# Optimization experiments

Measured on AMD Instinct MI355X. Metric: run time of the kernel, lower is better.

## Reference

```python
import jax, jax.numpy as jnp
import numpy as np

N = 100000   # nodes
E = 3200000  # edges
G = 256      # graphs in batch
C_IN, H, OUT = 5, 64, 2
EPS = 1e-5


def setup_inputs() -> dict:
    key = jax.random.key(0)
    ks = jax.random.split(key, 16)
    d = {
        "x": jax.random.normal(ks[0], (N, C_IN), jnp.float32),
        "edge_index": jax.random.randint(ks[1], (2, E), 0, N, jnp.int64),
        "batch": jnp.sort(jax.random.randint(ks[2], (N,), 0, G, jnp.int64)),
        "W1": jax.random.normal(ks[3], (C_IN, H), jnp.float32),
        "b1": jax.random.normal(ks[4], (H,), jnp.float32),
        "g1": jax.random.uniform(ks[5], (H,), jnp.float32),
        "be1": jax.random.normal(ks[6], (H,), jnp.float32),
        "rm1": jnp.zeros((H,), jnp.float32),
        "rv1": jnp.ones((H,), jnp.float32),
        "W2": jax.random.normal(ks[7], (H, H), jnp.float32),
        "b2": jax.random.normal(ks[8], (H,), jnp.float32),
        "g2": jax.random.uniform(ks[9], (H,), jnp.float32),
        "be2": jax.random.normal(ks[10], (H,), jnp.float32),
        "rm2": jnp.zeros((H,), jnp.float32),
        "rv2": jnp.ones((H,), jnp.float32),
        "W3": jax.random.normal(ks[11], (H, H), jnp.float32),
        "b3": jax.random.normal(ks[12], (H,), jnp.float32),
        "g3": jax.random.uniform(ks[13], (H,), jnp.float32),
        "be3": jax.random.normal(ks[14], (H,), jnp.float32),
        "rm3": jnp.zeros((H,), jnp.float32),
        "rv3": jnp.ones((H,), jnp.float32),
        "Wf1": jax.random.normal(ks[15], (H, 32), jnp.float32),
        "bf1": jax.random.normal(jax.random.fold_in(key, 1), (32,), jnp.float32),
        "Wf2": jax.random.normal(jax.random.fold_in(key, 2), (32, OUT), jnp.float32),
        "bf2": jax.random.normal(jax.random.fold_in(key, 3), (OUT,), jnp.float32),
    }
    return d


def reference(x, edge_index, batch, W1, b1, g1, be1, rm1, rv1,
              W2, b2, g2, be2, rm2, rv2, W3, b3, g3, be3, rm3, rv3,
              Wf1, bf1, Wf2, bf2):
    src, dst = edge_index[0], edge_index[1]
    # GCN symmetric normalization with self-loops: deg includes the self edge
    deg = jax.ops.segment_sum(jnp.ones((E,), x.dtype), dst, num_segments=N) + 1.0
    dinv = jax.lax.rsqrt(deg)            # [N]
    enorm = dinv[src] * dinv[dst]        # per-edge norm  [E]
    snorm = dinv * dinv                  # self-loop norm [N]

    def gcn(h, W, b):
        h = h @ W                                                  # [N,H]
        agg = jax.ops.segment_sum(h[src] * enorm[:, None], dst, num_segments=N)
        return agg + h * snorm[:, None] + b

    def bn(h, g, be, rm, rv):  # eval-mode BatchNorm1d
        return (h - rm) * jax.lax.rsqrt(rv + EPS) * g + be

    h = jax.nn.relu(bn(gcn(x, W1, b1), g1, be1, rm1, rv1))
    h = jax.nn.relu(bn(gcn(h, W2, b2), g2, be2, rm2, rv2))
    h = jax.nn.relu(bn(gcn(h, W3, b3), g3, be3, rm3, rv3))

    counts = jax.ops.segment_sum(jnp.ones((N,), h.dtype), batch, num_segments=G)
    pooled = jax.ops.segment_sum(h, batch, num_segments=G) / jnp.maximum(counts, 1.0)[:, None]

    h = jax.nn.relu(pooled @ Wf1 + bf1)  # dropout is identity in eval
    return jax.nn.sigmoid(h @ Wf2 + bf2)
```

## Files before the change

### kernel.cpp

```cpp
#include <hip/hip_runtime.h>
#include <hip/hip_bf16.h>

#define HF 64
#define EPS 1e-5f

#define BSH 9
#define BKN (1 << BSH)
#define NBUCK_MAX 256
#define PB_T 256
#define PB_EPT 32
#define PB_TILE (PB_T * PB_EPT)

#define LGRID 2048

typedef __hip_bfloat16 bf16;

__device__ __forceinline__ unsigned char f32_to_fp8(float v) {
    int p = __builtin_amdgcn_cvt_pk_fp8_f32(v, v, 0, false);
    return (unsigned char)(p & 0xff);
}

__device__ __forceinline__ float rdlane(float v, int k) {
    return __int_as_float(__builtin_amdgcn_readlane(__float_as_int(v), k));
}

__device__ __forceinline__ unsigned bf16_rne_hi(float x) {
    unsigned u = __float_as_uint(x);
    return (u + 0x7fffu + ((u >> 16) & 1u)) & 0xffff0000u;
}

__global__ __launch_bounds__(PB_T) void k_passB2(
    const int* __restrict__ src, const int* __restrict__ dst,
    int* __restrict__ stage, unsigned* __restrict__ rtab,
    int* __restrict__ bcnt, int E, int B) {
    __shared__ int scnt[NBUCK_MAX];
    __shared__ int sscan[PB_T];
    int t = threadIdx.x;
    int blk = blockIdx.x;
    int tile0 = blk * PB_TILE;

    for (int b = t; b < NBUCK_MAX; b += PB_T) scnt[b] = 0;
    __syncthreads();

    int rec[PB_EPT];
    int bkt[PB_EPT];
#pragma unroll
    for (int k = 0; k < PB_EPT; ++k) {
        int e = tile0 + k * PB_T + t;
        bkt[k] = -1;
        if (e < E) {
            int d = dst[e];
            int s = src[e];
            int b = d >> BSH;
            bkt[k] = b;
            rec[k] = s | ((d & (BKN - 1)) << 17);
            atomicAdd(&scnt[b], 1);
        }
    }
    __syncthreads();

    int v = (t < B) ? scnt[t] : 0;
    sscan[t] = v;
    __syncthreads();
    for (int off = 1; off < PB_T; off <<= 1) {
        int val = sscan[t];
        int add = (t >= off) ? sscan[t - off] : 0;
        __syncthreads();
        sscan[t] = val + add;
        __syncthreads();
    }
    int excl = sscan[t] - v;
    if (t < B) {
        rtab[(size_t)blk * B + t] = ((unsigned)excl << 14) | (unsigned)v;
        scnt[t] = excl;
        if (v) atomicAdd(&bcnt[t], v);
    }
    __syncthreads();

#pragma unroll
    for (int k = 0; k < PB_EPT; ++k) {
        if (bkt[k] >= 0) {
            int loc = atomicAdd(&scnt[bkt[k]], 1);
            stage[tile0 + loc] = rec[k];
        }
    }
}

__global__ void k_bscan3(const int* __restrict__ bcnt, int* __restrict__ bbase2,
                         int* __restrict__ base, int B, int N, int E) {
    __shared__ int tot[NBUCK_MAX];
    int t = threadIdx.x;
    int v = (t < B) ? bcnt[t] : 0;
    tot[t] = v;
    __syncthreads();
    for (int off = 1; off < 256; off <<= 1) {
        int val = tot[t];
        int add = (t >= off) ? tot[t - off] : 0;
        __syncthreads();
        tot[t] = val + add;
        __syncthreads();
    }
    if (t < B) bbase2[t] = tot[t] - v;
    if (t == 0) { bbase2[B] = E; base[N] = E; }
}

__global__ __launch_bounds__(512) void k_passC2(const int* __restrict__ stage,
                                                const unsigned* __restrict__ rtab,
                                                const int* __restrict__ bb2,
                                                const float* __restrict__ x,
                                                int* __restrict__ base,
                                                float* __restrict__ dinv,
                                                float* __restrict__ xs,
                                                int* __restrict__ csr,
                                                int N, int B, int nblk) {
    __shared__ int lcnt[BKN];
    __shared__ int lscan[BKN];
    __shared__ int lcur[BKN];
    int beta = blockIdx.x;
    int n0 = beta * BKN;
    int n1 = n0 + BKN; if (n1 > N) n1 = N;
    int nn = n1 - n0;
    int t = threadIdx.x;
    int rg = t >> 4;
    int le = t & 15;
    lcnt[t] = 0;
    __syncthreads();

    for (int blk0 = 0; blk0 < nblk; blk0 += 32) {
        int blk = blk0 + rg;
        if (blk < nblk) {
            unsigned rt = rtab[(size_t)blk * B + beta];
            int cnt = (int)(rt & 0x3FFFu);
            int off = blk * PB_TILE + (int)(rt >> 14);
            for (int i = le; i < cnt; i += 16)
                atomicAdd(&lcnt[stage[off + i] >> 17], 1);
        }
    }
    __syncthreads();
    int v = lcnt[t];
    lscan[t] = v;
    __syncthreads();
    for (int off = 1; off < 512; off <<= 1) {
        int val = lscan[t];
        int add = (t >= off) ? lscan[t - off] : 0;
        __syncthreads();
        lscan[t] = val + add;
        __syncthreads();
    }
    int b = bb2[beta] + lscan[t] - v;
    if (t < nn) {
        int n = n0 + t;
        float di = rsqrtf((float)v + 1.0f);
        base[n] = b;
        dinv[n] = di;
#pragma unroll
        for (int c2 = 0; c2 < 5; ++c2)
            xs[n * 5 + c2] = x[n * 5 + c2] * di;
    }
    lcur[t] = b;
    __syncthreads();

    for (int blk0 = 0; blk0 < nblk; blk0 += 32) {
        int blk = blk0 + rg;
        if (blk < nblk) {
            unsigned rt = rtab[(size_t)blk * B + beta];
            int cnt = (int)(rt & 0x3FFFu);
            int off = blk * PB_TILE + (int)(rt >> 14);
            for (int i = le; i < cnt; i += 16) {
                int r = stage[off + i];
                int pos = atomicAdd(&lcur[r >> 17], 1);
                csr[pos] = r & 0x1ffff;
            }
        }
    }
}

__global__ __launch_bounds__(256) void k_layer1(
    const float* __restrict__ xs, unsigned char* __restrict__ hout,
    const int* __restrict__ csr, const int* __restrict__ basep,
    const float* __restrict__ dinv,
    const float* __restrict__ W1, const float* __restrict__ b,
    const float* __restrict__ g, const float* __restrict__ be,
    const float* __restrict__ rm, const float* __restrict__ rv, int N) {
    __shared__ float sW[5 * HF];
    __shared__ float sB[HF];
    __shared__ float sScale[HF];
    if (threadIdx.x < HF) {
        int f = threadIdx.x;
        float scale = g[f] * rsqrtf(rv[f] + EPS);
        sScale[f] = scale;
        sB[f] = (b[f] - rm[f]) * scale + be[f];
    }
    __syncthreads();
    for (int i = threadIdx.x; i < 5 * HF; i += blockDim.x)
        sW[i] = W1[i] * sScale[i & (HF - 1)];
    __syncthreads();

    int lane = threadIdx.x & 63;
    int wave = threadIdx.x >> 6;
    int c  = lane & 7;
    int g8 = lane >> 3;
    int stride = gridDim.x * 4;

    auto mlp_store = [&](float accS, int nodeS, float diS) {
        float out = sB[lane];
#pragma unroll
        for (int k = 0; k < 5; ++k) out += __shfl(accS, k, 64) * sW[k * HF + lane];
        out = fmaxf(out, 0.f);
        hout[(size_t)nodeS * HF + lane] = f32_to_fp8(out * diS);
    };

    float accP = 0.f, diP = 0.f;
    int nodeP = -1;

    for (int node = blockIdx.x * 4 + wave; node < N; node += stride) {
        int j   = __builtin_amdgcn_readfirstlane(basep[node]);
        int end = __builtin_amdgcn_readfirstlane(basep[node + 1]);

        float a0 = 0.f, a1 = 0.f, a2 = 0.f, a3 = 0.f;
        if (g8 == 0 && c < 5) a0 = xs[node * 5 + c];

        float u0 = 0.f, u1 = 0.f, u2 = 0.f, u3 = 0.f;
        bool w0 = (j + 32 <= end);
        if (w0) {
            int s0 = csr[j + g8];
            int s1 = csr[j + 8 + g8];
            int s2 = csr[j + 16 + g8];
            int s3 = csr[j + 24 + g8];
            u0 = xs[s0 * 5 + c]; u1 = xs[s1 * 5 + c];
            u2 = xs[s2 * 5 + c]; u3 = xs[s3 * 5 + c];
        }

        if (nodeP >= 0) mlp_store(accP, nodeP, diP);

        if (w0) {
            j += 32;
            while (j + 32 <= end) {
                int s0 = csr[j + g8];
                int s1 = csr[j + 8 + g8];
                int s2 = csr[j + 16 + g8];
                int s3 = csr[j + 24 + g8];
                float v0 = xs[s0 * 5 + c];
                float v1 = xs[s1 * 5 + c];
                float v2 = xs[s2 * 5 + c];
                float v3 = xs[s3 * 5 + c];
                a0 += u0; a1 += u1; a2 += u2; a3 += u3;
                u0 = v0; u1 = v1; u2 = v2; u3 = v3;
                j += 32;
            }
            a0 += u0; a1 += u1; a2 += u2; a3 += u3;
        }
        for (; j + 8 <= end; j += 8) {
            int s = csr[j + g8];
            a0 += xs[s * 5 + c];
        }
        if (j < end && j + g8 < end) {
            int s = csr[j + g8];
            a0 += xs[s * 5 + c];
        }

        float acc = (a0 + a1) + (a2 + a3);
        acc += __shfl_xor(acc, 8, 64);
        acc += __shfl_xor(acc, 16, 64);
        acc += __shfl_xor(acc, 32, 64);

        float di = dinv[node];
        accP = acc * di;
        diP = di;
        nodeP = node;
    }
    if (nodeP >= 0) mlp_store(accP, nodeP, diP);
}

template <int SCALE_OUT>
__global__ __launch_bounds__(256, 4) void k_layer(
    const unsigned char* __restrict__ hs8, void* __restrict__ hout_v,
    const int* __restrict__ csr, const int* __restrict__ basep,
    const float* __restrict__ dinv,
    const float* __restrict__ W, const float* __restrict__ b,
    const float* __restrict__ g, const float* __restrict__ be,
    const float* __restrict__ rm, const float* __restrict__ rv, int N) {
    __shared__ uint4 swp4[64][9];

    int lane = threadIdx.x & 63;
    int wave = threadIdx.x >> 6;
    int stride = gridDim.x * 4;
    const unsigned char* col = hs8 + lane;

    if (threadIdx.x < 64) {
        int l = threadIdx.x;
        float sc = g[l] * rsqrtf(rv[l] + EPS);
#pragma unroll
        for (int c = 0; c < 8; ++c) {
            unsigned p[4];
#pragma unroll
            for (int q = 0; q < 4; ++q) {
                int k2 = c * 4 + q;
                unsigned lo = bf16_rne_hi(W[(2 * k2 + 0) * HF + l] * sc);
                unsigned hi = bf16_rne_hi(W[(2 * k2 + 1) * HF + l] * sc);
                p[q] = (lo >> 16) | hi;
            }
            swp4[l][c] = make_uint4(p[0], p[1], p[2], p[3]);
        }
    }
    __syncthreads();

    float scale = g[lane] * rsqrtf(rv[lane] + EPS);
    float bias  = (b[lane] - rm[lane]) * scale + be[lane];

    auto mlp_store = [&](float acc, int nodeS, float diS) {
        float o0 = bias, o1 = 0.f, o2 = 0.f, o3 = 0.f;
#pragma unroll
        for (int c = 0; c < 8; ++c) {
            uint4 pv = swp4[lane][c];
            int k0 = c * 8;
            o0 += rdlane(acc, k0 + 0) * __uint_as_float(pv.x << 16);
            o1 += rdlane(acc, k0 + 1) * __uint_as_float(pv.x & 0xffff0000u);
            o2 += rdlane(acc, k0 + 2) * __uint_as_float(pv.y << 16);
            o3 += rdlane(acc, k0 + 3) * __uint_as_float(pv.y & 0xffff0000u);
            o0 += rdlane(acc, k0 + 4) * __uint_as_float(pv.z << 16);
            o1 += rdlane(acc, k0 + 5) * __uint_as_float(pv.z & 0xffff0000u);
            o2 += rdlane(acc, k0 + 6) * __uint_as_float(pv.w << 16);
            o3 += rdlane(acc, k0 + 7) * __uint_as_float(pv.w & 0xffff0000u);
        }
        float out = fmaxf((o0 + o1) + (o2 + o3), 0.f);
        if (SCALE_OUT) {
            ((unsigned char*)hout_v)[(size_t)nodeS * HF + lane] = f32_to_fp8(out * diS);
        } else {
            ((unsigned short*)hout_v)[(size_t)nodeS * HF + lane] =
                (unsigned short)(bf16_rne_hi(out) >> 16);
        }
    };

    float accP = 0.f, diP = 0.f;
    int nodeP = -1;

    for (int node = blockIdx.x * 4 + wave; node < N; node += stride) {
        int j   = __builtin_amdgcn_readfirstlane(basep[node]);
        int end = __builtin_amdgcn_readfirstlane(basep[node + 1]);

        float a0 = __builtin_amdgcn_cvt_f32_fp8((unsigned)col[(size_t)node * HF], 0);
        float a1 = 0.f, a2 = 0.f, a3 = 0.f;

        unsigned u0 = 0, u1 = 0, u2 = 0, u3 = 0, u4 = 0, u5 = 0, u6 = 0, u7 = 0;
        bool w0 = (j + 8 <= end);
        if (w0) {
            int s0 = csr[j+0], s1 = csr[j+1], s2 = csr[j+2], s3 = csr[j+3];
            int s4 = csr[j+4], s5 = csr[j+5], s6 = csr[j+6], s7 = csr[j+7];
            u0 = col[(size_t)s0 * HF]; u1 = col[(size_t)s1 * HF];
            u2 = col[(size_t)s2 * HF]; u3 = col[(size_t)s3 * HF];
            u4 = col[(size_t)s4 * HF]; u5 = col[(size_t)s5 * HF];
            u6 = col[(size_t)s6 * HF]; u7 = col[(size_t)s7 * HF];
        }

        if (nodeP >= 0) mlp_store(accP, nodeP, diP);

        if (w0) {
            j += 8;
            while (j + 8 <= end) {
                int t0 = csr[j+0], t1 = csr[j+1], t2 = csr[j+2], t3 = csr[j+3];
                int t4 = csr[j+4], t5 = csr[j+5], t6 = csr[j+6], t7 = csr[j+7];
                unsigned v0 = col[(size_t)t0 * HF];
                unsigned v1 = col[(size_t)t1 * HF];
                unsigned v2 = col[(size_t)t2 * HF];
                unsigned v3 = col[(size_t)t3 * HF];
                unsigned v4 = col[(size_t)t4 * HF];
                unsigned v5 = col[(size_t)t5 * HF];
                unsigned v6 = col[(size_t)t6 * HF];
                unsigned v7 = col[(size_t)t7 * HF];
                a0 += __builtin_amdgcn_cvt_f32_fp8(u0, 0);
                a1 += __builtin_amdgcn_cvt_f32_fp8(u1, 0);
                a2 += __builtin_amdgcn_cvt_f32_fp8(u2, 0);
                a3 += __builtin_amdgcn_cvt_f32_fp8(u3, 0);
                a0 += __builtin_amdgcn_cvt_f32_fp8(u4, 0);
                a1 += __builtin_amdgcn_cvt_f32_fp8(u5, 0);
                a2 += __builtin_amdgcn_cvt_f32_fp8(u6, 0);
                a3 += __builtin_amdgcn_cvt_f32_fp8(u7, 0);
                u0 = v0; u1 = v1; u2 = v2; u3 = v3;
                u4 = v4; u5 = v5; u6 = v6; u7 = v7;
                j += 8;
            }
            a0 += __builtin_amdgcn_cvt_f32_fp8(u0, 0);
            a1 += __builtin_amdgcn_cvt_f32_fp8(u1, 0);
            a2 += __builtin_amdgcn_cvt_f32_fp8(u2, 0);
            a3 += __builtin_amdgcn_cvt_f32_fp8(u3, 0);
            a0 += __builtin_amdgcn_cvt_f32_fp8(u4, 0);
            a1 += __builtin_amdgcn_cvt_f32_fp8(u5, 0);
            a2 += __builtin_amdgcn_cvt_f32_fp8(u6, 0);
            a3 += __builtin_amdgcn_cvt_f32_fp8(u7, 0);
        }
        for (; j < end; ++j) {
            int s = csr[j];
            a0 += __builtin_amdgcn_cvt_f32_fp8((unsigned)col[(size_t)s * HF], 0);
        }

        float di = dinv[node];
        accP = ((a0 + a1) + (a2 + a3)) * di;
        diP = di;
        nodeP = node;
    }
    if (nodeP >= 0) mlp_store(accP, nodeP, diP);
}

__global__ void k_pool_fc(const unsigned short* __restrict__ h, const int* __restrict__ batch,
                          const float* __restrict__ Wf1, const float* __restrict__ bf1,
                          const float* __restrict__ Wf2, const float* __restrict__ bf2,
                          float* __restrict__ out, int N) {
    int g = blockIdx.x;
    int t = threadIdx.x;
    int f = t & 63, q = t >> 6;

    int lo = 0, hi = N;
    while (lo < hi) { int mid = (lo + hi) >> 1; if (batch[mid] < g) lo = mid + 1; else hi = mid; }
    int start = lo;
    hi = N;
    while (lo < hi) { int mid = (lo + hi) >> 1; if (batch[mid] < g + 1) lo = mid + 1; else hi = mid; }
    int end = lo;

    float sum = 0.f;
    for (int n = start + q; n < end; n += 4)
        sum += __uint_as_float(((unsigned)h[(size_t)n * HF + f]) << 16);

    __shared__ float red[4][HF];
    __shared__ float sp[HF];
    __shared__ float sh[32];
    red[q][f] = sum;
    __syncthreads();
    if (q == 0) {
        float s = red[0][f] + red[1][f] + red[2][f] + red[3][f];
        float cntf = (float)(end - start);
        sp[f] = s / fmaxf(cntf, 1.0f);
    }
    __syncthreads();
    if (t < 32) {
        float a = bf1[t];
#pragma unroll
        for (int k = 0; k < HF; ++k) a += sp[k] * Wf1[k * 32 + t];
        sh[t] = fmaxf(a, 0.f);
    }
    __syncthreads();
    if (t < 2) {
        float a = bf2[t];
#pragma unroll
        for (int k = 0; k < 32; ++k) a += sh[k] * Wf2[k * 2 + t];
        out[g * 2 + t] = 1.f / (1.f + expf(-a));
    }
}

extern "C" void kernel_launch(void* const* d_in, const int* in_sizes, int n_in,
                              void* d_out, int out_size, void* d_ws, size_t ws_size,
                              hipStream_t stream) {
    const float* x     = (const float*)d_in[0];
    const int*   ei    = (const int*)d_in[1];
    const int*   batch = (const int*)d_in[2];
    const float* W1 = (const float*)d_in[3];
    const float* b1 = (const float*)d_in[4];
    const float* g1 = (const float*)d_in[5];
    const float* be1 = (const float*)d_in[6];
    const float* rm1 = (const float*)d_in[7];
    const float* rv1 = (const float*)d_in[8];
    const float* W2 = (const float*)d_in[9];
    const float* b2 = (const float*)d_in[10];
    const float* g2 = (const float*)d_in[11];
    const float* be2 = (const float*)d_in[12];
    const float* rm2 = (const float*)d_in[13];
    const float* rv2 = (const float*)d_in[14];
    const float* W3 = (const float*)d_in[15];
    const float* b3 = (const float*)d_in[16];
    const float* g3 = (const float*)d_in[17];
    const float* be3 = (const float*)d_in[18];
    const float* rm3 = (const float*)d_in[19];
    const float* rv3 = (const float*)d_in[20];
    const float* Wf1 = (const float*)d_in[21];
    const float* bf1 = (const float*)d_in[22];
    const float* Wf2 = (const float*)d_in[23];
    const float* bf2 = (const float*)d_in[24];
    float* out = (float*)d_out;

    const int N = in_sizes[2];
    const int E = in_sizes[1] / 2;
    const int G = out_size / 2;
    const int B = (N + BKN - 1) / BKN;

    char* ws = (char*)d_ws;
    size_t off = 0;
    auto alloc = [&](size_t bytes) {
        char* p = ws + off;
        off += (bytes + 255) & ~(size_t)255;
        return p;
    };
    const int nblk = (E + PB_TILE - 1) / PB_TILE;

    size_t h3_bytes = (size_t)N * HF * 2;
    size_t st_bytes = (size_t)E * 4;
    unsigned short* H3 = (unsigned short*)alloc(h3_bytes > st_bytes ? h3_bytes : st_bytes);
    unsigned char* HS1      = (unsigned char*)alloc((size_t)N * HF);
    unsigned char* HS2      = (unsigned char*)alloc((size_t)N * HF);
    float*         xs       = (float*)alloc((size_t)N * 5 * sizeof(float) + 64);
    float*         dinv     = (float*)alloc((size_t)N * sizeof(float));
    int*           base     = (int*)  alloc(((size_t)N + 1) * sizeof(int));
    int*           bcnt     = (int*)  alloc((size_t)NBUCK_MAX * sizeof(int));
    int*           bbase2   = (int*)  alloc(((size_t)NBUCK_MAX + 1) * sizeof(int));
    unsigned*      rtab     = (unsigned*)alloc((size_t)nblk * B * sizeof(unsigned));
    int*           csr      = (int*)  alloc((size_t)E * sizeof(int));
    int*           stage    = (int*)H3;

    const int* src = ei;
    const int* dst = ei + E;

    const int BT = 256;

    hipMemsetAsync(bcnt, 0, (size_t)B * sizeof(int), stream);
    k_passB2<<<nblk, PB_T, 0, stream>>>(src, dst, stage, rtab, bcnt, E, B);
    k_bscan3<<<1, 256, 0, stream>>>(bcnt, bbase2, base, B, N, E);
    k_passC2<<<B, 512, 0, stream>>>(stage, rtab, bbase2, x, base, dinv, xs, csr, N, B, nblk);

    k_layer1<<<LGRID, BT, 0, stream>>>(xs, HS1, csr, base, dinv,
                                       W1, b1, g1, be1, rm1, rv1, N);
    k_layer<1><<<LGRID, BT, 0, stream>>>(HS1, HS2, csr, base, dinv,
                                         W2, b2, g2, be2, rm2, rv2, N);
    k_layer<0><<<LGRID, BT, 0, stream>>>(HS2, H3, csr, base, dinv,
                                         W3, b3, g3, be3, rm3, rv3, N);

    k_pool_fc<<<G, BT, 0, stream>>>(H3, batch, Wf1, bf1, Wf2, bf2, out, N);
}
```

Before: 414.0 us.

## Replace readlane dense transform with MFMA bf16 over 16-node tiles per wave

Layers 2 and 3 now gather 16 nodes per wave, stage the aggregated rows in LDS as bf16, and apply the 64x64 weight with MFMA 16x16x32 bf16 instructions instead of 64 readlane-FMA steps per node. Weights are held in registers as MFMA B fragments with the batchnorm scale folded in. The launch grid changes from a fixed persistent grid to one block per 64 nodes, and the old overlap of the MLP step with the next node's gather is removed. Output stores become scattered by row/column from the MFMA layout, which may reduce store coalescing, and register pressure rises.

```diff
diff --git a/kernel.cpp b/kernel.cpp
--- a/kernel.cpp
+++ b/kernel.cpp
@@ -14,14 +14,12 @@
 #define LGRID 2048
 
 typedef __hip_bfloat16 bf16;
+typedef short bf16x8 __attribute__((ext_vector_type(8)));
+typedef float f32x4 __attribute__((ext_vector_type(4)));
 
 __device__ __forceinline__ unsigned char f32_to_fp8(float v) {
     int p = __builtin_amdgcn_cvt_pk_fp8_f32(v, v, 0, false);
     return (unsigned char)(p & 0xff);
-}
-
-__device__ __forceinline__ float rdlane(float v, int k) {
-    return __int_as_float(__builtin_amdgcn_readlane(__float_as_int(v), k));
 }
 
 __device__ __forceinline__ unsigned bf16_rne_hi(float x) {
@@ -280,94 +278,78 @@
     const float* __restrict__ W, const float* __restrict__ b,
     const float* __restrict__ g, const float* __restrict__ be,
     const float* __restrict__ rm, const float* __restrict__ rv, int N) {
-    __shared__ uint4 swp4[64][9];
+    __shared__ __align__(16) short Alds[4][16 * 72];
+    __shared__ float dlds[4][16];
 
     int lane = threadIdx.x & 63;
     int wave = threadIdx.x >> 6;
-    int stride = gridDim.x * 4;
+    int nb = blockIdx.x * 64 + wave * 16;
     const unsigned char* col = hs8 + lane;
 
-    if (threadIdx.x < 64) {
-        int l = threadIdx.x;
-        float sc = g[l] * rsqrtf(rv[l] + EPS);
-#pragma unroll
-        for (int c = 0; c < 8; ++c) {
-            unsigned p[4];
-#pragma unroll
-            for (int q = 0; q < 4; ++q) {
-                int k2 = c * 4 + q;
-                unsigned lo = bf16_rne_hi(W[(2 * k2 + 0) * HF + l] * sc);
-                unsigned hi = bf16_rne_hi(W[(2 * k2 + 1) * HF + l] * sc);
-                p[q] = (lo >> 16) | hi;
-            }
-            swp4[l][c] = make_uint4(p[0], p[1], p[2], p[3]);
-        }
-    }
-    __syncthreads();
-
-    float scale = g[lane] * rsqrtf(rv[lane] + EPS);
-    float bias  = (b[lane] - rm[lane]) * scale + be[lane];
-
-    auto mlp_store = [&](float acc, int nodeS, float diS) {
-        float o0 = bias, o1 = 0.f, o2 = 0.f, o3 = 0.f;
-#pragma unroll
-        for (int c = 0; c < 8; ++c) {
-            uint4 pv = swp4[lane][c];
-            int k0 = c * 8;
-            o0 += rdlane(acc, k0 + 0) * __uint_as_float(pv.x << 16);
-            o1 += rdlane(acc, k0 + 1) * __uint_as_float(pv.x & 0xffff0000u);
-            o2 += rdlane(acc, k0 + 2) * __uint_as_float(pv.y << 16);
-            o3 += rdlane(acc, k0 + 3) * __uint_as_float(pv.y & 0xffff0000u);
-            o0 += rdlane(acc, k0 + 4) * __uint_as_float(pv.z << 16);
-            o1 += rdlane(acc, k0 + 5) * __uint_as_float(pv.z & 0xffff0000u);
-            o2 += rdlane(acc, k0 + 6) * __uint_as_float(pv.w << 16);
-            o3 += rdlane(acc, k0 + 7) * __uint_as_float(pv.w & 0xffff0000u);
-        }
-        float out = fmaxf((o0 + o1) + (o2 + o3), 0.f);
-        if (SCALE_OUT) {
-            ((unsigned char*)hout_v)[(size_t)nodeS * HF + lane] = f32_to_fp8(out * diS);
-        } else {
-            ((unsigned short*)hout_v)[(size_t)nodeS * HF + lane] =
-                (unsigned short)(bf16_rne_hi(out) >> 16);
-        }
-    };
-
-    float accP = 0.f, diP = 0.f;
-    int nodeP = -1;
-
-    for (int node = blockIdx.x * 4 + wave; node < N; node += stride) {
-        int j   = __builtin_amdgcn_readfirstlane(basep[node]);
-        int end = __builtin_amdgcn_readfirstlane(basep[node + 1]);
-
-        float a0 = __builtin_amdgcn_cvt_f32_fp8((unsigned)col[(size_t)node * HF], 0);
-        float a1 = 0.f, a2 = 0.f, a3 = 0.f;
-
-        unsigned u0 = 0, u1 = 0, u2 = 0, u3 = 0, u4 = 0, u5 = 0, u6 = 0, u7 = 0;
-        bool w0 = (j + 8 <= end);
-        if (w0) {
-            int s0 = csr[j+0], s1 = csr[j+1], s2 = csr[j+2], s3 = csr[j+3];
-            int s4 = csr[j+4], s5 = csr[j+5], s6 = csr[j+6], s7 = csr[j+7];
-            u0 = col[(size_t)s0 * HF]; u1 = col[(size_t)s1 * HF];
-            u2 = col[(size_t)s2 * HF]; u3 = col[(size_t)s3 * HF];
-            u4 = col[(size_t)s4 * HF]; u5 = col[(size_t)s5 * HF];
-            u6 = col[(size_t)s6 * HF]; u7 = col[(size_t)s7 * HF];
-        }
-
-        if (nodeP >= 0) mlp_store(accP, nodeP, diP);
-
-        if (w0) {
-            j += 8;
-            while (j + 8 <= end) {
-                int t0 = csr[j+0], t1 = csr[j+1], t2 = csr[j+2], t3 = csr[j+3];
-                int t4 = csr[j+4], t5 = csr[j+5], t6 = csr[j+6], t7 = csr[j+7];
-                unsigned v0 = col[(size_t)t0 * HF];
-                unsigned v1 = col[(size_t)t1 * HF];
-                unsigned v2 = col[(size_t)t2 * HF];
-                unsigned v3 = col[(size_t)t3 * HF];
-                unsigned v4 = col[(size_t)t4 * HF];
-                unsigned v5 = col[(size_t)t5 * HF];
-                unsigned v6 = col[(size_t)t6 * HF];
-                unsigned v7 = col[(size_t)t7 * HF];
+    int row  = lane & 15;
+    int quad = lane >> 4;
+
+    bf16x8 Bf[4][2];
+    float bias4[4];
+#pragma unroll
+    for (int t = 0; t < 4; ++t) {
+        int n = t * 16 + row;
+        float sc = g[n] * rsqrtf(rv[n] + EPS);
+        bias4[t] = (b[n] - rm[n]) * sc + be[n];
+#pragma unroll
+        for (int kh = 0; kh < 2; ++kh)
+#pragma unroll
+            for (int e = 0; e < 8; ++e) {
+                int k = quad * 8 + kh * 32 + e;
+                Bf[t][kh][e] = (short)(bf16_rne_hi(W[k * HF + n] * sc) >> 16);
+            }
+    }
+
+    for (int i = 0; i < 16; ++i) {
+        int node = nb + i;
+        float acc = 0.f;
+        if (node < N) {
+            int j   = __builtin_amdgcn_readfirstlane(basep[node]);
+            int end = __builtin_amdgcn_readfirstlane(basep[node + 1]);
+
+            float a0 = __builtin_amdgcn_cvt_f32_fp8((unsigned)col[(size_t)node * HF], 0);
+            float a1 = 0.f, a2 = 0.f, a3 = 0.f;
+
+            unsigned u0 = 0, u1 = 0, u2 = 0, u3 = 0, u4 = 0, u5 = 0, u6 = 0, u7 = 0;
+            bool w0 = (j + 8 <= end);
+            if (w0) {
+                int s0 = csr[j+0], s1 = csr[j+1], s2 = csr[j+2], s3 = csr[j+3];
+                int s4 = csr[j+4], s5 = csr[j+5], s6 = csr[j+6], s7 = csr[j+7];
+                u0 = col[(size_t)s0 * HF]; u1 = col[(size_t)s1 * HF];
+                u2 = col[(size_t)s2 * HF]; u3 = col[(size_t)s3 * HF];
+                u4 = col[(size_t)s4 * HF]; u5 = col[(size_t)s5 * HF];
+                u6 = col[(size_t)s6 * HF]; u7 = col[(size_t)s7 * HF];
+            }
+            if (w0) {
+                j += 8;
+                while (j + 8 <= end) {
+                    int t0 = csr[j+0], t1 = csr[j+1], t2 = csr[j+2], t3 = csr[j+3];
+                    int t4 = csr[j+4], t5 = csr[j+5], t6 = csr[j+6], t7 = csr[j+7];
+                    unsigned v0 = col[(size_t)t0 * HF];
+                    unsigned v1 = col[(size_t)t1 * HF];
+                    unsigned v2 = col[(size_t)t2 * HF];
+                    unsigned v3 = col[(size_t)t3 * HF];
+                    unsigned v4 = col[(size_t)t4 * HF];
+                    unsigned v5 = col[(size_t)t5 * HF];
+                    unsigned v6 = col[(size_t)t6 * HF];
+                    unsigned v7 = col[(size_t)t7 * HF];
+                    a0 += __builtin_amdgcn_cvt_f32_fp8(u0, 0);
+                    a1 += __builtin_amdgcn_cvt_f32_fp8(u1, 0);
+                    a2 += __builtin_amdgcn_cvt_f32_fp8(u2, 0);
+                    a3 += __builtin_amdgcn_cvt_f32_fp8(u3, 0);
+                    a0 += __builtin_amdgcn_cvt_f32_fp8(u4, 0);
+                    a1 += __builtin_amdgcn_cvt_f32_fp8(u5, 0);
+                    a2 += __builtin_amdgcn_cvt_f32_fp8(u6, 0);
+                    a3 += __builtin_amdgcn_cvt_f32_fp8(u7, 0);
+                    u0 = v0; u1 = v1; u2 = v2; u3 = v3;
+                    u4 = v4; u5 = v5; u6 = v6; u7 = v7;
+                    j += 8;
+                }
                 a0 += __builtin_amdgcn_cvt_f32_fp8(u0, 0);
                 a1 += __builtin_amdgcn_cvt_f32_fp8(u1, 0);
                 a2 += __builtin_amdgcn_cvt_f32_fp8(u2, 0);
@@ -376,30 +358,48 @@
                 a1 += __builtin_amdgcn_cvt_f32_fp8(u5, 0);
                 a2 += __builtin_amdgcn_cvt_f32_fp8(u6, 0);
                 a3 += __builtin_amdgcn_cvt_f32_fp8(u7, 0);
-                u0 = v0; u1 = v1; u2 = v2; u3 = v3;
-                u4 = v4; u5 = v5; u6 = v6; u7 = v7;
-                j += 8;
-            }
-            a0 += __builtin_amdgcn_cvt_f32_fp8(u0, 0);
-            a1 += __builtin_amdgcn_cvt_f32_fp8(u1, 0);
-            a2 += __builtin_amdgcn_cvt_f32_fp8(u2, 0);
-            a3 += __builtin_amdgcn_cvt_f32_fp8(u3, 0);
-            a0 += __builtin_amdgcn_cvt_f32_fp8(u4, 0);
-            a1 += __builtin_amdgcn_cvt_f32_fp8(u5, 0);
-            a2 += __builtin_amdgcn_cvt_f32_fp8(u6, 0);
-            a3 += __builtin_amdgcn_cvt_f32_fp8(u7, 0);
-        }
-        for (; j < end; ++j) {
-            int s = csr[j];
-            a0 += __builtin_amdgcn_cvt_f32_fp8((unsigned)col[(size_t)s * HF], 0);
-        }
-
-        float di = dinv[node];
-        accP = ((a0 + a1) + (a2 + a3)) * di;
-        diP = di;
-        nodeP = node;
-    }
-    if (nodeP >= 0) mlp_store(accP, nodeP, diP);
+            }
+            for (; j < end; ++j) {
+                int s = csr[j];
+                a0 += __builtin_amdgcn_cvt_f32_fp8((unsigned)col[(size_t)s * HF], 0);
+            }
+            float di = dinv[node];
+            acc = ((a0 + a1) + (a2 + a3)) * di;
+            if (SCALE_OUT && lane == 0) dlds[wave][i] = di;
+        }
+        Alds[wave][i * 72 + lane] = (short)(bf16_rne_hi(acc) >> 16);
+    }
+
+    const short* ap = &Alds[wave][0];
+    bf16x8 A0 = *(const bf16x8*)(ap + row * 72 + quad * 8);
+    bf16x8 A1 = *(const bf16x8*)(ap + row * 72 + quad * 8 + 32);
+
+    float d4[4];
+    if (SCALE_OUT) {
+#pragma unroll
+        for (int jj = 0; jj < 4; ++jj) d4[jj] = dlds[wave][quad * 4 + jj];
+    }
+
+#pragma unroll
+    for (int t = 0; t < 4; ++t) {
+        f32x4 acc = {0.f, 0.f, 0.f, 0.f};
+        acc = __builtin_amdgcn_mfma_f32_16x16x32_bf16(A0, Bf[t][0], acc, 0, 0, 0);
+        acc = __builtin_amdgcn_mfma_f32_16x16x32_bf16(A1, Bf[t][1], acc, 0, 0, 0);
+#pragma unroll
+        for (int jj = 0; jj < 4; ++jj) {
+            int noder = nb + quad * 4 + jj;
+            float o = fmaxf(acc[jj] + bias4[t], 0.f);
+            if (noder < N) {
+                if (SCALE_OUT) {
+                    ((unsigned char*)hout_v)[(size_t)noder * HF + t * 16 + row] =
+                        f32_to_fp8(o * d4[jj]);
+                } else {
+                    ((unsigned short*)hout_v)[(size_t)noder * HF + t * 16 + row] =
+                        (unsigned short)(bf16_rne_hi(o) >> 16);
+                }
+            }
+        }
+    }
 }
 
 __global__ void k_pool_fc(const unsigned short* __restrict__ h, const int* __restrict__ batch,
@@ -515,12 +515,13 @@
     k_bscan3<<<1, 256, 0, stream>>>(bcnt, bbase2, base, B, N, E);
     k_passC2<<<B, 512, 0, stream>>>(stage, rtab, bbase2, x, base, dinv, xs, csr, N, B, nblk);
 
+    int gl = (N + 63) / 64;
     k_layer1<<<LGRID, BT, 0, stream>>>(xs, HS1, csr, base, dinv,
                                        W1, b1, g1, be1, rm1, rv1, N);
-    k_layer<1><<<LGRID, BT, 0, stream>>>(HS1, HS2, csr, base, dinv,
-                                         W2, b2, g2, be2, rm2, rv2, N);
-    k_layer<0><<<LGRID, BT, 0, stream>>>(HS2, H3, csr, base, dinv,
-                                         W3, b3, g3, be3, rm3, rv3, N);
+    k_layer<1><<<gl, BT, 0, stream>>>(HS1, HS2, csr, base, dinv,
+                                      W2, b2, g2, be2, rm2, rv2, N);
+    k_layer<0><<<gl, BT, 0, stream>>>(HS2, H3, csr, base, dinv,
+                                      W3, b3, g3, be3, rm3, rv3, N);
 
     k_pool_fc<<<G, BT, 0, stream>>>(H3, batch, Wf1, bf1, Wf2, bf2, out, N);
 }
```

Result: slower. 528.4 us (+27.6%).
